# Kernel tuning notes

Measured on AMD Instinct MI355X. Metric: run time of the kernel, lower is better.

The kernel has to match this reference:

```python
import jax, jax.numpy as jnp
import numpy as np

IN_DIM, BANDS = 42, 22
H_VAD, H_NOISE, H_DEN = 24, 48, 96


def gru(x, w_ih, w_hh, b_ih, b_hh):
    """torch.nn.GRU (batch_first) semantics, h0=0.
    x: [B,T,D]; w_ih: [3H,D]; w_hh: [3H,H]; gate order r,z,n."""
    H = w_hh.shape[1]
    # precompute input projections for all timesteps (big GEMM, recurrence only on H)
    xp = jnp.einsum('btd,gd->btg', x, w_ih) + b_ih  # [B,T,3H]

    def step(h, xt):
        hp = h @ w_hh.T + b_hh
        xr, xz, xn = jnp.split(xt, 3, axis=-1)
        hr, hz, hn = jnp.split(hp, 3, axis=-1)
        r = jax.nn.sigmoid(xr + hr)
        z = jax.nn.sigmoid(xz + hz)
        n = jnp.tanh(xn + r * hn)
        h_new = (1.0 - z) * n + z * h
        return h_new, h_new

    h0 = jnp.zeros((x.shape[0], H), x.dtype)
    _, hs = jax.lax.scan(step, h0, jnp.swapaxes(xp, 0, 1))  # [T,B,H]
    return jnp.swapaxes(hs, 0, 1)  # [B,T,H]


def setup_inputs() -> dict:
    key = jax.random.key(0)
    ks = jax.random.split(key, 20)

    def w(k, shape, fan):
        return (jax.random.normal(k, shape, jnp.float32) / np.sqrt(fan)).astype(jnp.float32)

    B, T = 256, 2000
    d_noise_in = H_VAD + H_VAD + IN_DIM     # 90
    d_den_in = H_VAD + H_NOISE + IN_DIM     # 114
    return {
        'x': jax.random.normal(ks[0], (B, T, IN_DIM), jnp.float32),
        'in_w': w(ks[1], (H_VAD, IN_DIM), IN_DIM),
        'in_b': jnp.zeros((H_VAD,), jnp.float32),
        'vad_wih': w(ks[2], (3 * H_VAD, H_VAD), H_VAD),
        'vad_whh': w(ks[3], (3 * H_VAD, H_VAD), H_VAD),
        'vad_bih': jnp.zeros((3 * H_VAD,), jnp.float32),
        'vad_bhh': jnp.zeros((3 * H_VAD,), jnp.float32),
        'vad_out_w': w(ks[4], (1, H_VAD), H_VAD),
        'vad_out_b': jnp.zeros((1,), jnp.float32),
        'noise_wih': w(ks[5], (3 * H_NOISE, d_noise_in), d_noise_in),
        'noise_whh': w(ks[6], (3 * H_NOISE, H_NOISE), H_NOISE),
        'noise_bih': jnp.zeros((3 * H_NOISE,), jnp.float32),
        'noise_bhh': jnp.zeros((3 * H_NOISE,), jnp.float32),
        'den_wih': w(ks[7], (3 * H_DEN, d_den_in), d_den_in),
        'den_whh': w(ks[8], (3 * H_DEN, H_DEN), H_DEN),
        'den_bih': jnp.zeros((3 * H_DEN,), jnp.float32),
        'den_bhh': jnp.zeros((3 * H_DEN,), jnp.float32),
        'out_w': w(ks[9], (BANDS, H_DEN), H_DEN),
        'out_b': jnp.zeros((BANDS,), jnp.float32),
    }


def reference(x, in_w, in_b, vad_wih, vad_whh, vad_bih, vad_bhh,
              vad_out_w, vad_out_b, noise_wih, noise_whh, noise_bih, noise_bhh,
              den_wih, den_whh, den_bih, den_bhh, out_w, out_b):
    tmp = jnp.tanh(jnp.einsum('btd,hd->bth', x, in_w) + in_b)          # [B,T,24]
    vad_h = gru(tmp, vad_wih, vad_whh, vad_bih, vad_bhh)               # [B,T,24]
    vad = jax.nn.sigmoid(jnp.einsum('bth,oh->bto', vad_h, vad_out_w) + vad_out_b)
    noise_in = jnp.concatenate([tmp, vad_h, x], axis=-1)               # [B,T,90]
    noise_h = gru(noise_in, noise_wih, noise_whh, noise_bih, noise_bhh)  # [B,T,48]
    den_in = jnp.concatenate([vad_h, noise_h, x], axis=-1)             # [B,T,114]
    den_h = gru(den_in, den_wih, den_whh, den_bih, den_bhh)            # [B,T,96]
    gains = jax.nn.sigmoid(jnp.einsum('bth,oh->bto', den_h, out_w) + out_b)
    return gains, vad
```

## Files before the change

kernel.cpp:

```cpp
#include <hip/hip_runtime.h>

typedef _Float16 f16;
typedef _Float16 h2 __attribute__((ext_vector_type(2)));
typedef unsigned int u32;

#define TB  256
#define TTT 2000
#define INW 42
#define HV  24
#define HN  48
#define HD  96
#define NTH 640

__device__ __forceinline__ float fsigm(float v) {
    return __builtin_amdgcn_rcpf(1.0f + __builtin_amdgcn_exp2f(-1.44269504089f * v));
}
__device__ __forceinline__ float ftanh(float v) {
    float e = __builtin_amdgcn_exp2f(2.88539008178f * v);
    return 1.0f - 2.0f * __builtin_amdgcn_rcpf(e + 1.0f);
}
__device__ __forceinline__ float dot2f(u32 a, u32 w, float c) {
#if __has_builtin(__builtin_amdgcn_fdot2)
    return __builtin_amdgcn_fdot2(__builtin_bit_cast(h2, a), __builtin_bit_cast(h2, w), c, false);
#else
    h2 av = __builtin_bit_cast(h2, a), wv = __builtin_bit_cast(h2, w);
    return c + (float)av[0] * (float)wv[0] + (float)av[1] * (float)wv[1];
#endif
}
__device__ __forceinline__ u32 packw(float a, float b) {
    h2 v; v[0] = (f16)a; v[1] = (f16)b;
    return __builtin_bit_cast(u32, v);
}
template<int CTRL>
__device__ __forceinline__ float dpp_add(float x) {
    int y = __builtin_amdgcn_mov_dpp(__builtin_bit_cast(int, x), CTRL, 0xF, 0xF, true);
    return x + __builtin_bit_cast(float, y);
}

#define SYNCB() asm volatile("s_waitcnt lgkmcnt(0)\n\ts_barrier" ::: "memory")

#define ACCI(AV, W, IDX) do { u32 _a = (AV); \
    rr = dot2f(_a, W[0][IDX], rr); zz = dot2f(_a, W[1][IDX], zz); an = dot2f(_a, W[2][IDX], an); } while (0)
#define ACCH(AV, W, IDX) do { u32 _a = (AV); \
    rr = dot2f(_a, W[0][IDX], rr); zz = dot2f(_a, W[1][IDX], zz); hn = dot2f(_a, W[2][IDX], hn); } while (0)
#define RED4_Q() do { \
    rr = dpp_add<0xB1>(rr); rr = dpp_add<0x4E>(rr); \
    zz = dpp_add<0xB1>(zz); zz = dpp_add<0x4E>(zz); \
    an = dpp_add<0xB1>(an); an = dpp_add<0x4E>(an); \
    hn = dpp_add<0xB1>(hn); hn = dpp_add<0x4E>(hn); } while (0)
#define RED4_1() do { \
    rr = dpp_add<0xB1>(rr); zz = dpp_add<0xB1>(zz); \
    an = dpp_add<0xB1>(an); hn = dpp_add<0xB1>(hn); } while (0)

template<int N> struct IC { static constexpr int val = N; };

__global__ __launch_bounds__(NTH, 3) void rnnoise_kernel(
    const float* __restrict__ gx,
    const float* __restrict__ in_w,      const float* __restrict__ in_b,
    const float* __restrict__ vad_wih,   const float* __restrict__ vad_whh,
    const float* __restrict__ vad_bih,   const float* __restrict__ vad_bhh,
    const float* __restrict__ vad_out_w, const float* __restrict__ vad_out_b,
    const float* __restrict__ noise_wih, const float* __restrict__ noise_whh,
    const float* __restrict__ noise_bih, const float* __restrict__ noise_bhh,
    const float* __restrict__ den_wih,   const float* __restrict__ den_whh,
    const float* __restrict__ den_bih,   const float* __restrict__ den_bhh,
    const float* __restrict__ out_w,     const float* __restrict__ out_b,
    float* __restrict__ gains, float* __restrict__ vout)
{
    __shared__ __align__(16) f16 s_x[4][48];
    __shared__ __align__(16) f16 s_tmp[4][24];
    __shared__ __align__(16) f16 s_vadh[4][24];
    __shared__ __align__(16) f16 s_noih[4][48];
    __shared__ __align__(16) f16 s_denh[4][96];

    const int tid  = threadIdx.x;
    const int wid  = tid >> 6;
    const int lane = tid & 63;
    const int b    = blockIdx.x;

    if (tid < 96)  ((u32*)s_x)[tid]    = 0u;
    if (tid < 48)  ((u32*)s_tmp)[tid]  = 0u;
    if (tid < 48)  ((u32*)s_vadh)[tid] = 0u;
    if (tid < 96)  ((u32*)s_noih)[tid] = 0u;
    if (tid < 192) ((u32*)s_denh)[tid] = 0u;
    __syncthreads();

    const int role = (wid == 9) ? 2 : ((wid == 4 || wid == 5 || wid == 8) ? 1 : 0);

    if (role == 0) {
        const int dwi = (wid < 4) ? wid : (wid - 2);
        const int u = dwi * 16 + (lane >> 2), q = lane & 3;
        u32 wdh[3][12], wdx[3][6], wdv[3][3], wdn[3][6];
        #pragma unroll
        for (int g = 0; g < 3; ++g) {
            const float* wr = den_whh + (g * HD + u) * HD + 24 * q;
            #pragma unroll
            for (int j = 0; j < 12; ++j) wdh[g][j] = packw(wr[2*j], wr[2*j+1]);
            const float* wi = den_wih + (g * HD + u) * 114;
            #pragma unroll
            for (int j = 0; j < 6; ++j) {
                int c0 = 12*q + 2*j;
                float a = (c0     < INW) ? wi[72 + c0]     : 0.f;
                float c = (c0 + 1 < INW) ? wi[72 + c0 + 1] : 0.f;
                wdx[g][j] = packw(a, c);
            }
            #pragma unroll
            for (int j = 0; j < 3; ++j) wdv[g][j] = packw(wi[6*q + 2*j], wi[6*q + 2*j + 1]);
            #pragma unroll
            for (int j = 0; j < 6; ++j) wdn[g][j] = packw(wi[24 + 12*q + 2*j], wi[24 + 12*q + 2*j + 1]);
        }
        const float bdr  = den_bih[u]      + den_bhh[u];
        const float bdz  = den_bih[HD+u]   + den_bhh[HD+u];
        const float bdni = den_bih[2*HD+u];
        const float bdnh = den_bhh[2*HD+u];
        float hreg = 0.f;

        auto step = [&](auto PC, int k) {
            constexpr int P  = decltype(PC)::val;
            constexpr int SI = (P + 1) & 3;
            if (k >= 3 && k <= TTT + 2) {
                float rr = 0, zz = 0, an = 0, hn = 0;
                const uint4* hp = (const uint4*)&s_denh[P][24*q];
                #pragma unroll
                for (int v = 0; v < 3; ++v) {
                    uint4 a = hp[v];
                    ACCH(a.x, wdh, 4*v+0); ACCH(a.y, wdh, 4*v+1);
                    ACCH(a.z, wdh, 4*v+2); ACCH(a.w, wdh, 4*v+3);
                }
                const uint2* xp = (const uint2*)&s_x[SI][12*q];
                #pragma unroll
                for (int v = 0; v < 3; ++v) { uint2 a = xp[v]; ACCI(a.x, wdx, 2*v); ACCI(a.y, wdx, 2*v+1); }
                const u32* vp = (const u32*)&s_vadh[SI][6*q];
                #pragma unroll
                for (int v = 0; v < 3; ++v) ACCI(vp[v], wdv, v);
                const uint2* np = (const uint2*)&s_noih[SI][12*q];
                #pragma unroll
                for (int v = 0; v < 3; ++v) { uint2 a = np[v]; ACCI(a.x, wdn, 2*v); ACCI(a.y, wdn, 2*v+1); }
                RED4_Q();
                if (q == 0) {
                    float r = fsigm(rr + bdr);
                    float z = fsigm(zz + bdz);
                    float n = ftanh(an + bdni + r * (hn + bdnh));
                    hreg = z * (hreg - n) + n;
                    s_denh[SI][u] = (f16)hreg;
                }
            }
            SYNCB();
        };
        #pragma clang loop unroll(disable)
        for (int k0 = 0; k0 < TTT + 4; k0 += 4) {
            step(IC<0>{}, k0); step(IC<1>{}, k0+1); step(IC<2>{}, k0+2); step(IC<3>{}, k0+3);
        }

    } else if (role == 1) {
        const int nwi = (wid == 4) ? 0 : ((wid == 5) ? 1 : 2);
        const int L = nwi * 64 + lane, u = L >> 2, q = L & 3;
        const int o = L >> 3, s8 = L & 7;
        const int oc = (o < 22) ? o : 0;
        u32 wnh[3][6], wnt[3][3], wnv[3][3], wnx[3][6], wo[6];
        #pragma unroll
        for (int g = 0; g < 3; ++g) {
            const float* wr = noise_whh + (g * HN + u) * HN + 12 * q;
            #pragma unroll
            for (int j = 0; j < 6; ++j) wnh[g][j] = packw(wr[2*j], wr[2*j+1]);
            const float* wi = noise_wih + (g * HN + u) * 90;
            #pragma unroll
            for (int j = 0; j < 3; ++j) wnt[g][j] = packw(wi[6*q + 2*j], wi[6*q + 2*j + 1]);
            #pragma unroll
            for (int j = 0; j < 3; ++j) wnv[g][j] = packw(wi[24 + 6*q + 2*j], wi[24 + 6*q + 2*j + 1]);
            #pragma unroll
            for (int j = 0; j < 6; ++j) {
                int c0 = 12*q + 2*j;
                float a = (c0     < INW) ? wi[48 + c0]     : 0.f;
                float c = (c0 + 1 < INW) ? wi[48 + c0 + 1] : 0.f;
                wnx[g][j] = packw(a, c);
            }
        }
        #pragma unroll
        for (int j = 0; j < 6; ++j) wo[j] = packw(out_w[oc*HD + 12*s8 + 2*j], out_w[oc*HD + 12*s8 + 2*j + 1]);
        const float bnr  = noise_bih[u]    + noise_bhh[u];
        const float bnz  = noise_bih[HN+u] + noise_bhh[HN+u];
        const float bnni = noise_bih[2*HN+u];
        const float bnnh = noise_bhh[2*HN+u];
        const float bo   = out_b[oc];
        float hreg = 0.f;

        auto step = [&](auto PC, int k) {
            constexpr int P  = decltype(PC)::val;
            constexpr int SI = (P + 2) & 3;
            constexpr int SH = (P + 1) & 3;
            if (k >= 2 && k <= TTT + 1) {
                float rr = 0, zz = 0, an = 0, hn = 0;
                const uint2* hp = (const uint2*)&s_noih[SH][12*q];
                #pragma unroll
                for (int v = 0; v < 3; ++v) { uint2 a = hp[v]; ACCH(a.x, wnh, 2*v); ACCH(a.y, wnh, 2*v+1); }
                const u32* tp = (const u32*)&s_tmp[SI][6*q];
                #pragma unroll
                for (int v = 0; v < 3; ++v) ACCI(tp[v], wnt, v);
                const u32* vp = (const u32*)&s_vadh[SI][6*q];
                #pragma unroll
                for (int v = 0; v < 3; ++v) ACCI(vp[v], wnv, v);
                const uint2* xp = (const uint2*)&s_x[SI][12*q];
                #pragma unroll
                for (int v = 0; v < 3; ++v) { uint2 a = xp[v]; ACCI(a.x, wnx, 2*v); ACCI(a.y, wnx, 2*v+1); }
                RED4_Q();
                if (q == 0) {
                    float r = fsigm(rr + bnr);
                    float z = fsigm(zz + bnz);
                    float n = ftanh(an + bnni + r * (hn + bnnh));
                    hreg = z * (hreg - n) + n;
                    s_noih[SI][u] = (f16)hreg;
                }
            }
            if (k >= 4) {
                float acc = 0;
                const uint2* dp = (const uint2*)&s_denh[P][12*s8];
                #pragma unroll
                for (int v = 0; v < 3; ++v) {
                    uint2 a = dp[v];
                    acc = dot2f(a.x, wo[2*v], acc); acc = dot2f(a.y, wo[2*v+1], acc);
                }
                acc = dpp_add<0xB1>(acc); acc = dpp_add<0x4E>(acc);
                acc += __shfl_xor(acc, 4);
                if (s8 == 0 && o < 22)
                    gains[((size_t)b * TTT + (k - 4)) * 22 + o] = fsigm(acc + bo);
            }
            SYNCB();
        };
        #pragma clang loop unroll(disable)
        for (int k0 = 0; k0 < TTT + 4; k0 += 4) {
            step(IC<0>{}, k0); step(IC<1>{}, k0+1); step(IC<2>{}, k0+2); step(IC<3>{}, k0+3);
        }

    } else {
        const int l = lane;
        const int u = (l < 48) ? (l >> 1) : 0, q2 = l & 1;
        u32 wvi[3][6], wvh[3][6], wtm[12];
        float bvr = 0, bvz = 0, bvni = 0, bvnh = 0, btm = 0, wvo_u = 0;
        if (l < 48) {
            #pragma unroll
            for (int g = 0; g < 3; ++g) {
                const float* wi = vad_wih + (g * HV + u) * HV + 12 * q2;
                const float* wh = vad_whh + (g * HV + u) * HV + 12 * q2;
                #pragma unroll
                for (int j = 0; j < 6; ++j) {
                    wvi[g][j] = packw(wi[2*j], wi[2*j+1]);
                    wvh[g][j] = packw(wh[2*j], wh[2*j+1]);
                }
            }
            #pragma unroll
            for (int j = 0; j < 12; ++j) {
                int c0 = 24*q2 + 2*j;
                float a = (c0     < INW) ? in_w[u*INW + c0]     : 0.f;
                float c = (c0 + 1 < INW) ? in_w[u*INW + c0 + 1] : 0.f;
                wtm[j] = packw(a, c);
            }
            bvr  = vad_bih[u]      + vad_bhh[u];
            bvz  = vad_bih[HV+u]   + vad_bhh[HV+u];
            bvni = vad_bih[2*HV+u];
            bvnh = vad_bhh[2*HV+u];
            btm  = in_b[u];
            if (q2 == 0) wvo_u = vad_out_w[u];
        }
        const float bvo = vad_out_b[0];
        float hreg = 0.f;

        float xa = 0, xb = 0, xc = 0, xd = 0;
        if (l < INW) {
            xa = gx[((size_t)b * TTT + 0) * INW + l];
            xb = gx[((size_t)b * TTT + 1) * INW + l];
            xc = gx[((size_t)b * TTT + 2) * INW + l];
            xd = gx[((size_t)b * TTT + 3) * INW + l];
        }

        auto step = [&](auto PC, int k) {
            constexpr int P  = decltype(PC)::val;
            constexpr int ST = (P + 3) & 3;
            constexpr int SH = (P + 2) & 3;
            if (k < TTT && l < INW) {
                float xv;
                if constexpr (P == 0) xv = xa; else if constexpr (P == 1) xv = xb;
                else if constexpr (P == 2) xv = xc; else xv = xd;
                s_x[P][l] = (f16)xv;
            }
            if (k + 4 < TTT && l < INW) {
                float xv = gx[((size_t)b * TTT + (k + 4)) * INW + l];
                if constexpr (P == 0) xa = xv; else if constexpr (P == 1) xb = xv;
                else if constexpr (P == 2) xc = xv; else xd = xv;
            }
            if (k >= 1 && k <= TTT) {
                float rr = 0, zz = 0, an = 0, hn = 0;
                if (l < 48) {
                    const uint2* tp = (const uint2*)&s_tmp[ST][12*q2];
                    const uint2* hp = (const uint2*)&s_vadh[SH][12*q2];
                    #pragma unroll
                    for (int v = 0; v < 3; ++v) {
                        uint2 a = tp[v]; ACCI(a.x, wvi, 2*v); ACCI(a.y, wvi, 2*v+1);
                        uint2 h = hp[v]; ACCH(h.x, wvh, 2*v); ACCH(h.y, wvh, 2*v+1);
                    }
                    RED4_1();
                    if (q2 == 0) {
                        float r = fsigm(rr + bvr);
                        float z = fsigm(zz + bvz);
                        float n = ftanh(an + bvni + r * (hn + bvnh));
                        hreg = z * (hreg - n) + n;
                        s_vadh[ST][u] = (f16)hreg;
                    }
                }
                float val = (l < 48 && q2 == 0) ? (wvo_u * hreg) : 0.f;
                val = dpp_add<0xB1>(val); val = dpp_add<0x4E>(val);
                val += __shfl_xor(val, 4); val += __shfl_xor(val, 8);
                val += __shfl_xor(val, 16); val += __shfl_xor(val, 32);
                if (l == 0) vout[(size_t)b * TTT + (k - 1)] = fsigm(val + bvo);
            }
            if (k < TTT) {
                float acc = 0;
                if (l < 48) {
                    const uint4* xp = (const uint4*)&s_x[P][24*q2];
                    #pragma unroll
                    for (int v = 0; v < 3; ++v) {
                        uint4 a = xp[v];
                        acc = dot2f(a.x, wtm[4*v+0], acc); acc = dot2f(a.y, wtm[4*v+1], acc);
                        acc = dot2f(a.z, wtm[4*v+2], acc); acc = dot2f(a.w, wtm[4*v+3], acc);
                    }
                    acc = dpp_add<0xB1>(acc);
                    if (q2 == 0) s_tmp[P][u] = (f16)ftanh(acc + btm);
                }
            }
            SYNCB();
        };
        #pragma clang loop unroll(disable)
        for (int k0 = 0; k0 < TTT + 4; k0 += 4) {
            step(IC<0>{}, k0); step(IC<1>{}, k0+1); step(IC<2>{}, k0+2); step(IC<3>{}, k0+3);
        }
    }
}

extern "C" void kernel_launch(void* const* d_in, const int* in_sizes, int n_in,
                              void* d_out, int out_size, void* d_ws, size_t ws_size,
                              hipStream_t stream) {
    (void)in_sizes; (void)n_in; (void)d_ws; (void)ws_size; (void)out_size;
    const float* gx        = (const float*)d_in[0];
    const float* in_w      = (const float*)d_in[1];
    const float* in_b      = (const float*)d_in[2];
    const float* vad_wih   = (const float*)d_in[3];
    const float* vad_whh   = (const float*)d_in[4];
    const float* vad_bih   = (const float*)d_in[5];
    const float* vad_bhh   = (const float*)d_in[6];
    const float* vad_out_w = (const float*)d_in[7];
    const float* vad_out_b = (const float*)d_in[8];
    const float* noise_wih = (const float*)d_in[9];
    const float* noise_whh = (const float*)d_in[10];
    const float* noise_bih = (const float*)d_in[11];
    const float* noise_bhh = (const float*)d_in[12];
    const float* den_wih   = (const float*)d_in[13];
    const float* den_whh   = (const float*)d_in[14];
    const float* den_bih   = (const float*)d_in[15];
    const float* den_bhh   = (const float*)d_in[16];
    const float* out_w     = (const float*)d_in[17];
    const float* out_b     = (const float*)d_in[18];
    float* gains = (float*)d_out;
    float* vout  = (float*)d_out + (size_t)TB * (size_t)TTT * 22;

    rnnoise_kernel<<<dim3(TB), dim3(NTH), 0, stream>>>(
        gx, in_w, in_b, vad_wih, vad_whh, vad_bih, vad_bhh, vad_out_w, vad_out_b,
        noise_wih, noise_whh, noise_bih, noise_bhh, den_wih, den_whh, den_bih, den_bhh,
        out_w, out_b, gains, vout);
}
```

Before: 1.923 ms.

## Compute noise and denoise GRU gate projections with MFMA on unified activation buffer

The noise and denoise GRU steps now use 16x16x32 f16 MFMA instructions instead of per-lane fdot2 chains with DPP reductions. All activations move into one contiguous shared buffer so the concatenated input can be read as B-fragments, and the output gain projection moves from the noise waves into two denoise waves, also on MFMA. The MFMA B operand is a single batch column broadcast across 16 columns, so most of the matrix work is redundant, and launch bounds drop to one block per SM to make room for the larger register weight fragments.

After: 2.364 ms. 1.23x slower.

```diff
diff --git a/kernel.cpp b/kernel.cpp
--- a/kernel.cpp
+++ b/kernel.cpp
@@ -2,6 +2,8 @@
 
 typedef _Float16 f16;
 typedef _Float16 h2 __attribute__((ext_vector_type(2)));
+typedef _Float16 f16x8 __attribute__((ext_vector_type(8)));
+typedef float f32x4 __attribute__((ext_vector_type(4)));
 typedef unsigned int u32;
 
 #define TB  256
@@ -12,6 +14,13 @@
 #define HD  96
 #define NTH 640
 
+#define C_TMP 0
+#define C_VAD 24
+#define C_X   48
+#define C_NOI 96
+#define C_DEN 160
+#define ACTW  256
+
 __device__ __forceinline__ float fsigm(float v) {
     return __builtin_amdgcn_rcpf(1.0f + __builtin_amdgcn_exp2f(-1.44269504089f * v));
 }
@@ -39,22 +48,24 @@
 
 #define SYNCB() asm volatile("s_waitcnt lgkmcnt(0)\n\ts_barrier" ::: "memory")
 
+#define MFMA16(A, B, C) __builtin_amdgcn_mfma_f32_16x16x32_f16((A), (B), (C), 0, 0, 0)
+
 #define ACCI(AV, W, IDX) do { u32 _a = (AV); \
     rr = dot2f(_a, W[0][IDX], rr); zz = dot2f(_a, W[1][IDX], zz); an = dot2f(_a, W[2][IDX], an); } while (0)
 #define ACCH(AV, W, IDX) do { u32 _a = (AV); \
     rr = dot2f(_a, W[0][IDX], rr); zz = dot2f(_a, W[1][IDX], zz); hn = dot2f(_a, W[2][IDX], hn); } while (0)
-#define RED4_Q() do { \
-    rr = dpp_add<0xB1>(rr); rr = dpp_add<0x4E>(rr); \
-    zz = dpp_add<0xB1>(zz); zz = dpp_add<0x4E>(zz); \
-    an = dpp_add<0xB1>(an); an = dpp_add<0x4E>(an); \
-    hn = dpp_add<0xB1>(hn); hn = dpp_add<0x4E>(hn); } while (0)
 #define RED4_1() do { \
     rr = dpp_add<0xB1>(rr); zz = dpp_add<0xB1>(zz); \
     an = dpp_add<0xB1>(an); hn = dpp_add<0xB1>(hn); } while (0)
 
 template<int N> struct IC { static constexpr int val = N; };
 
-__global__ __launch_bounds__(NTH, 3) void rnnoise_kernel(
+__device__ __forceinline__ f16x8 ldsb(const f16* p) {
+    uint4 t = *(const uint4*)p;
+    return __builtin_bit_cast(f16x8, t);
+}
+
+__global__ __launch_bounds__(NTH, 1) void rnnoise_kernel(
     const float* __restrict__ gx,
     const float* __restrict__ in_w,      const float* __restrict__ in_b,
     const float* __restrict__ vad_wih,   const float* __restrict__ vad_whh,
@@ -67,82 +78,113 @@
     const float* __restrict__ out_w,     const float* __restrict__ out_b,
     float* __restrict__ gains, float* __restrict__ vout)
 {
-    __shared__ __align__(16) f16 s_x[4][48];
-    __shared__ __align__(16) f16 s_tmp[4][24];
-    __shared__ __align__(16) f16 s_vadh[4][24];
-    __shared__ __align__(16) f16 s_noih[4][48];
-    __shared__ __align__(16) f16 s_denh[4][96];
+    __shared__ __align__(16) f16 act[4][ACTW];
 
     const int tid  = threadIdx.x;
     const int wid  = tid >> 6;
     const int lane = tid & 63;
     const int b    = blockIdx.x;
-
-    if (tid < 96)  ((u32*)s_x)[tid]    = 0u;
-    if (tid < 48)  ((u32*)s_tmp)[tid]  = 0u;
-    if (tid < 48)  ((u32*)s_vadh)[tid] = 0u;
-    if (tid < 96)  ((u32*)s_noih)[tid] = 0u;
-    if (tid < 192) ((u32*)s_denh)[tid] = 0u;
-    __syncthreads();
+    const int g4   = lane >> 4;
+    const int rrow = lane & 15;
+
+    if (tid < 512) ((u32*)act)[tid] = 0u;
 
     const int role = (wid == 9) ? 2 : ((wid == 4 || wid == 5 || wid == 8) ? 1 : 0);
 
     if (role == 0) {
         const int dwi = (wid < 4) ? wid : (wid - 2);
-        const int u = dwi * 16 + (lane >> 2), q = lane & 3;
-        u32 wdh[3][12], wdx[3][6], wdv[3][3], wdn[3][6];
+        const int u_a = 16 * dwi + rrow;
+        f16x8 ag[3][7];
         #pragma unroll
         for (int g = 0; g < 3; ++g) {
-            const float* wr = den_whh + (g * HD + u) * HD + 24 * q;
+            const float* wi = den_wih + (g * HD + u_a) * 114;
+            const float* wh = den_whh + (g * HD + u_a) * HD;
             #pragma unroll
-            for (int j = 0; j < 12; ++j) wdh[g][j] = packw(wr[2*j], wr[2*j+1]);
-            const float* wi = den_wih + (g * HD + u) * 114;
+            for (int kt = 0; kt < 7; ++kt) {
+                #pragma unroll
+                for (int j = 0; j < 8; ++j) {
+                    int k = (kt < 4) ? (32 * kt + 8 * g4 + j) : (128 + 32 * (kt - 4) + 8 * g4 + j);
+                    float w = 0.f;
+                    if (k < 24)        w = wi[k];
+                    else if (k < 66)   w = wi[72 + (k - 24)];
+                    else if (k < 72)   w = 0.f;
+                    else if (k < 120)  w = wi[24 + (k - 72)];
+                    else if (k < 128)  w = 0.f;
+                    else               w = wh[k - 128];
+                    ag[g][kt][j] = (f16)w;
+                }
+            }
+        }
+        f16x8 ao0 = {}, ao1 = {}, ao2 = {};
+        if (dwi < 2) {
+            int o = 16 * dwi + rrow;
             #pragma unroll
-            for (int j = 0; j < 6; ++j) {
-                int c0 = 12*q + 2*j;
-                float a = (c0     < INW) ? wi[72 + c0]     : 0.f;
-                float c = (c0 + 1 < INW) ? wi[72 + c0 + 1] : 0.f;
-                wdx[g][j] = packw(a, c);
-            }
-            #pragma unroll
-            for (int j = 0; j < 3; ++j) wdv[g][j] = packw(wi[6*q + 2*j], wi[6*q + 2*j + 1]);
-            #pragma unroll
-            for (int j = 0; j < 6; ++j) wdn[g][j] = packw(wi[24 + 12*q + 2*j], wi[24 + 12*q + 2*j + 1]);
-        }
-        const float bdr  = den_bih[u]      + den_bhh[u];
-        const float bdz  = den_bih[HD+u]   + den_bhh[HD+u];
-        const float bdni = den_bih[2*HD+u];
-        const float bdnh = den_bhh[2*HD+u];
-        float hreg = 0.f;
+            for (int j = 0; j < 8; ++j) {
+                ao0[j] = (f16)((o < 22) ? out_w[o * HD +  0 + 8 * g4 + j] : 0.f);
+                ao1[j] = (f16)((o < 22) ? out_w[o * HD + 32 + 8 * g4 + j] : 0.f);
+                ao2[j] = (f16)((o < 22) ? out_w[o * HD + 64 + 8 * g4 + j] : 0.f);
+            }
+        }
+        float bdr[4], bdz[4], bdni[4], bdnh[4], bog[4];
+        #pragma unroll
+        for (int i = 0; i < 4; ++i) {
+            int u = 16 * dwi + 4 * g4 + i;
+            bdr[i]  = den_bih[u]        + den_bhh[u];
+            bdz[i]  = den_bih[HD + u]   + den_bhh[HD + u];
+            bdni[i] = den_bih[2*HD + u];
+            bdnh[i] = den_bhh[2*HD + u];
+            int o = 16 * dwi + 4 * g4 + i;
+            bog[i] = (dwi < 2 && o < 22) ? out_b[o] : 0.f;
+        }
+        float hprev[4] = {0.f, 0.f, 0.f, 0.f};
+        __syncthreads();
 
         auto step = [&](auto PC, int k) {
             constexpr int P  = decltype(PC)::val;
             constexpr int SI = (P + 1) & 3;
+            f16x8 bh0 = ldsb(&act[P][C_DEN +  0 + 8 * g4]);
+            f16x8 bh1 = ldsb(&act[P][C_DEN + 32 + 8 * g4]);
+            f16x8 bh2 = ldsb(&act[P][C_DEN + 64 + 8 * g4]);
             if (k >= 3 && k <= TTT + 2) {
-                float rr = 0, zz = 0, an = 0, hn = 0;
-                const uint4* hp = (const uint4*)&s_denh[P][24*q];
-                #pragma unroll
-                for (int v = 0; v < 3; ++v) {
-                    uint4 a = hp[v];
-                    ACCH(a.x, wdh, 4*v+0); ACCH(a.y, wdh, 4*v+1);
-                    ACCH(a.z, wdh, 4*v+2); ACCH(a.w, wdh, 4*v+3);
-                }
-                const uint2* xp = (const uint2*)&s_x[SI][12*q];
-                #pragma unroll
-                for (int v = 0; v < 3; ++v) { uint2 a = xp[v]; ACCI(a.x, wdx, 2*v); ACCI(a.y, wdx, 2*v+1); }
-                const u32* vp = (const u32*)&s_vadh[SI][6*q];
-                #pragma unroll
-                for (int v = 0; v < 3; ++v) ACCI(vp[v], wdv, v);
-                const uint2* np = (const uint2*)&s_noih[SI][12*q];
-                #pragma unroll
-                for (int v = 0; v < 3; ++v) { uint2 a = np[v]; ACCI(a.x, wdn, 2*v); ACCI(a.y, wdn, 2*v+1); }
-                RED4_Q();
-                if (q == 0) {
-                    float r = fsigm(rr + bdr);
-                    float z = fsigm(zz + bdz);
-                    float n = ftanh(an + bdni + r * (hn + bdnh));
-                    hreg = z * (hreg - n) + n;
-                    s_denh[SI][u] = (f16)hreg;
+                f16x8 b0 = ldsb(&act[SI][24 +  0 + 8 * g4]);
+                f16x8 b1 = ldsb(&act[SI][24 + 32 + 8 * g4]);
+                f16x8 b2 = ldsb(&act[SI][24 + 64 + 8 * g4]);
+                f16x8 b3 = ldsb(&act[SI][24 + 96 + 8 * g4]);
+                f32x4 aR = {0,0,0,0}, aZ = {0,0,0,0}, aNi = {0,0,0,0}, aNh = {0,0,0,0};
+                aR = MFMA16(ag[0][0], b0, aR); aZ = MFMA16(ag[1][0], b0, aZ); aNi = MFMA16(ag[2][0], b0, aNi);
+                aR = MFMA16(ag[0][1], b1, aR); aZ = MFMA16(ag[1][1], b1, aZ); aNi = MFMA16(ag[2][1], b1, aNi);
+                aR = MFMA16(ag[0][2], b2, aR); aZ = MFMA16(ag[1][2], b2, aZ); aNi = MFMA16(ag[2][2], b2, aNi);
+                aR = MFMA16(ag[0][3], b3, aR); aZ = MFMA16(ag[1][3], b3, aZ); aNi = MFMA16(ag[2][3], b3, aNi);
+                aR = MFMA16(ag[0][4], bh0, aR); aZ = MFMA16(ag[1][4], bh0, aZ); aNh = MFMA16(ag[2][4], bh0, aNh);
+                aR = MFMA16(ag[0][5], bh1, aR); aZ = MFMA16(ag[1][5], bh1, aZ); aNh = MFMA16(ag[2][5], bh1, aNh);
+                aR = MFMA16(ag[0][6], bh2, aR); aZ = MFMA16(ag[1][6], bh2, aZ); aNh = MFMA16(ag[2][6], bh2, aNh);
+                #pragma unroll
+                for (int i = 0; i < 4; ++i) {
+                    float r = fsigm(aR[i] + bdr[i]);
+                    float z = fsigm(aZ[i] + bdz[i]);
+                    float n = ftanh(aNi[i] + bdni[i] + r * (aNh[i] + bdnh[i]));
+                    hprev[i] = z * (hprev[i] - n) + n;
+                }
+                if ((lane & 15) == 0) {
+                    h2 p0, p1;
+                    p0[0] = (f16)hprev[0]; p0[1] = (f16)hprev[1];
+                    p1[0] = (f16)hprev[2]; p1[1] = (f16)hprev[3];
+                    uint2 w; w.x = __builtin_bit_cast(u32, p0); w.y = __builtin_bit_cast(u32, p1);
+                    *(uint2*)&act[SI][C_DEN + 16 * dwi + 4 * g4] = w;
+                }
+            }
+            if (dwi < 2 && k >= 4) {
+                f32x4 aO = {0,0,0,0};
+                aO = MFMA16(ao0, bh0, aO);
+                aO = MFMA16(ao1, bh1, aO);
+                aO = MFMA16(ao2, bh2, aO);
+                if ((lane & 15) == 0) {
+                    #pragma unroll
+                    for (int i = 0; i < 4; ++i) {
+                        int o = 16 * dwi + 4 * g4 + i;
+                        if (o < 22)
+                            gains[((size_t)b * TTT + (k - 4)) * 22 + o] = fsigm(aO[i] + bog[i]);
+                    }
                 }
             }
             SYNCB();
@@ -154,76 +196,68 @@
 
     } else if (role == 1) {
         const int nwi = (wid == 4) ? 0 : ((wid == 5) ? 1 : 2);
-        const int L = nwi * 64 + lane, u = L >> 2, q = L & 3;
-        const int o = L >> 3, s8 = L & 7;
-        const int oc = (o < 22) ? o : 0;
-        u32 wnh[3][6], wnt[3][3], wnv[3][3], wnx[3][6], wo[6];
+        const int u_a = 16 * nwi + rrow;
+        f16x8 ag[3][5];
         #pragma unroll
         for (int g = 0; g < 3; ++g) {
-            const float* wr = noise_whh + (g * HN + u) * HN + 12 * q;
+            const float* wi = noise_wih + (g * HN + u_a) * 90;
+            const float* wh = noise_whh + (g * HN + u_a) * HN;
             #pragma unroll
-            for (int j = 0; j < 6; ++j) wnh[g][j] = packw(wr[2*j], wr[2*j+1]);
-            const float* wi = noise_wih + (g * HN + u) * 90;
-            #pragma unroll
-            for (int j = 0; j < 3; ++j) wnt[g][j] = packw(wi[6*q + 2*j], wi[6*q + 2*j + 1]);
-            #pragma unroll
-            for (int j = 0; j < 3; ++j) wnv[g][j] = packw(wi[24 + 6*q + 2*j], wi[24 + 6*q + 2*j + 1]);
-            #pragma unroll
-            for (int j = 0; j < 6; ++j) {
-                int c0 = 12*q + 2*j;
-                float a = (c0     < INW) ? wi[48 + c0]     : 0.f;
-                float c = (c0 + 1 < INW) ? wi[48 + c0 + 1] : 0.f;
-                wnx[g][j] = packw(a, c);
-            }
-        }
+            for (int kt = 0; kt < 5; ++kt) {
+                #pragma unroll
+                for (int j = 0; j < 8; ++j) {
+                    int k = (kt < 3) ? (32 * kt + 8 * g4 + j) : (96 + 32 * (kt - 3) + 8 * g4 + j);
+                    float w = 0.f;
+                    if (k < 90)       w = wi[k];
+                    else if (k < 96)  w = 0.f;
+                    else if (k < 144) w = wh[k - 96];
+                    else              w = 0.f;
+                    ag[g][kt][j] = (f16)w;
+                }
+            }
+        }
+        float bnr[4], bnz[4], bnni[4], bnnh[4];
         #pragma unroll
-        for (int j = 0; j < 6; ++j) wo[j] = packw(out_w[oc*HD + 12*s8 + 2*j], out_w[oc*HD + 12*s8 + 2*j + 1]);
-        const float bnr  = noise_bih[u]    + noise_bhh[u];
-        const float bnz  = noise_bih[HN+u] + noise_bhh[HN+u];
-        const float bnni = noise_bih[2*HN+u];
-        const float bnnh = noise_bhh[2*HN+u];
-        const float bo   = out_b[oc];
-        float hreg = 0.f;
+        for (int i = 0; i < 4; ++i) {
+            int u = 16 * nwi + 4 * g4 + i;
+            bnr[i]  = noise_bih[u]        + noise_bhh[u];
+            bnz[i]  = noise_bih[HN + u]   + noise_bhh[HN + u];
+            bnni[i] = noise_bih[2*HN + u];
+            bnnh[i] = noise_bhh[2*HN + u];
+        }
+        float hprev[4] = {0.f, 0.f, 0.f, 0.f};
+        __syncthreads();
 
         auto step = [&](auto PC, int k) {
-            constexpr int P  = decltype(PC)::val;
-            constexpr int SI = (P + 2) & 3;
-            constexpr int SH = (P + 1) & 3;
+            constexpr int P   = decltype(PC)::val;
+            constexpr int SI2 = (P + 2) & 3;
+            constexpr int SH  = (P + 1) & 3;
             if (k >= 2 && k <= TTT + 1) {
-                float rr = 0, zz = 0, an = 0, hn = 0;
-                const uint2* hp = (const uint2*)&s_noih[SH][12*q];
-                #pragma unroll
-                for (int v = 0; v < 3; ++v) { uint2 a = hp[v]; ACCH(a.x, wnh, 2*v); ACCH(a.y, wnh, 2*v+1); }
-                const u32* tp = (const u32*)&s_tmp[SI][6*q];
-                #pragma unroll
-                for (int v = 0; v < 3; ++v) ACCI(tp[v], wnt, v);
-                const u32* vp = (const u32*)&s_vadh[SI][6*q];
-                #pragma unroll
-                for (int v = 0; v < 3; ++v) ACCI(vp[v], wnv, v);
-                const uint2* xp = (const uint2*)&s_x[SI][12*q];
-                #pragma unroll
-                for (int v = 0; v < 3; ++v) { uint2 a = xp[v]; ACCI(a.x, wnx, 2*v); ACCI(a.y, wnx, 2*v+1); }
-                RED4_Q();
-                if (q == 0) {
-                    float r = fsigm(rr + bnr);
-                    float z = fsigm(zz + bnz);
-                    float n = ftanh(an + bnni + r * (hn + bnnh));
-                    hreg = z * (hreg - n) + n;
-                    s_noih[SI][u] = (f16)hreg;
-                }
-            }
-            if (k >= 4) {
-                float acc = 0;
-                const uint2* dp = (const uint2*)&s_denh[P][12*s8];
-                #pragma unroll
-                for (int v = 0; v < 3; ++v) {
-                    uint2 a = dp[v];
-                    acc = dot2f(a.x, wo[2*v], acc); acc = dot2f(a.y, wo[2*v+1], acc);
-                }
-                acc = dpp_add<0xB1>(acc); acc = dpp_add<0x4E>(acc);
-                acc += __shfl_xor(acc, 4);
-                if (s8 == 0 && o < 22)
-                    gains[((size_t)b * TTT + (k - 4)) * 22 + o] = fsigm(acc + bo);
+                f16x8 b0  = ldsb(&act[SI2][ 0 + 8 * g4]);
+                f16x8 b1  = ldsb(&act[SI2][32 + 8 * g4]);
+                f16x8 b2  = ldsb(&act[SI2][64 + 8 * g4]);
+                f16x8 bh0 = ldsb(&act[SH][C_NOI +  0 + 8 * g4]);
+                f16x8 bh1 = ldsb(&act[SH][C_NOI + 32 + 8 * g4]);
+                f32x4 aR = {0,0,0,0}, aZ = {0,0,0,0}, aNi = {0,0,0,0}, aNh = {0,0,0,0};
+                aR = MFMA16(ag[0][0], b0, aR); aZ = MFMA16(ag[1][0], b0, aZ); aNi = MFMA16(ag[2][0], b0, aNi);
+                aR = MFMA16(ag[0][1], b1, aR); aZ = MFMA16(ag[1][1], b1, aZ); aNi = MFMA16(ag[2][1], b1, aNi);
+                aR = MFMA16(ag[0][2], b2, aR); aZ = MFMA16(ag[1][2], b2, aZ); aNi = MFMA16(ag[2][2], b2, aNi);
+                aR = MFMA16(ag[0][3], bh0, aR); aZ = MFMA16(ag[1][3], bh0, aZ); aNh = MFMA16(ag[2][3], bh0, aNh);
+                aR = MFMA16(ag[0][4], bh1, aR); aZ = MFMA16(ag[1][4], bh1, aZ); aNh = MFMA16(ag[2][4], bh1, aNh);
+                #pragma unroll
+                for (int i = 0; i < 4; ++i) {
+                    float r = fsigm(aR[i] + bnr[i]);
+                    float z = fsigm(aZ[i] + bnz[i]);
+                    float n = ftanh(aNi[i] + bnni[i] + r * (aNh[i] + bnnh[i]));
+                    hprev[i] = z * (hprev[i] - n) + n;
+                }
+                if ((lane & 15) == 0) {
+                    h2 p0, p1;
+                    p0[0] = (f16)hprev[0]; p0[1] = (f16)hprev[1];
+                    p1[0] = (f16)hprev[2]; p1[1] = (f16)hprev[3];
+                    uint2 w; w.x = __builtin_bit_cast(u32, p0); w.y = __builtin_bit_cast(u32, p1);
+                    *(uint2*)&act[SI2][C_NOI + 16 * nwi + 4 * g4] = w;
+                }
             }
             SYNCB();
         };
@@ -250,15 +284,15 @@
             }
             #pragma unroll
             for (int j = 0; j < 12; ++j) {
-                int c0 = 24*q2 + 2*j;
-                float a = (c0     < INW) ? in_w[u*INW + c0]     : 0.f;
-                float c = (c0 + 1 < INW) ? in_w[u*INW + c0 + 1] : 0.f;
+                int c0 = 24 * q2 + 2 * j;
+                float a = (c0     < INW) ? in_w[u * INW + c0]     : 0.f;
+                float c = (c0 + 1 < INW) ? in_w[u * INW + c0 + 1] : 0.f;
                 wtm[j] = packw(a, c);
             }
-            bvr  = vad_bih[u]      + vad_bhh[u];
-            bvz  = vad_bih[HV+u]   + vad_bhh[HV+u];
-            bvni = vad_bih[2*HV+u];
-            bvnh = vad_bhh[2*HV+u];
+            bvr  = vad_bih[u]        + vad_bhh[u];
+            bvz  = vad_bih[HV + u]   + vad_bhh[HV + u];
+            bvni = vad_bih[2*HV + u];
+            bvnh = vad_bhh[2*HV + u];
             btm  = in_b[u];
             if (q2 == 0) wvo_u = vad_out_w[u];
         }
@@ -272,6 +306,7 @@
             xc = gx[((size_t)b * TTT + 2) * INW + l];
             xd = gx[((size_t)b * TTT + 3) * INW + l];
         }
+        __syncthreads();
 
         auto step = [&](auto PC, int k) {
             constexpr int P  = decltype(PC)::val;
@@ -281,7 +316,7 @@
                 float xv;
                 if constexpr (P == 0) xv = xa; else if constexpr (P == 1) xv = xb;
                 else if constexpr (P == 2) xv = xc; else xv = xd;
-                s_x[P][l] = (f16)xv;
+                act[P][C_X + l] = (f16)xv;
             }
             if (k + 4 < TTT && l < INW) {
                 float xv = gx[((size_t)b * TTT + (k + 4)) * INW + l];
@@ -291,8 +326,8 @@
             if (k >= 1 && k <= TTT) {
                 float rr = 0, zz = 0, an = 0, hn = 0;
                 if (l < 48) {
-                    const uint2* tp = (const uint2*)&s_tmp[ST][12*q2];
-                    const uint2* hp = (const uint2*)&s_vadh[SH][12*q2];
+                    const uint2* tp = (const uint2*)&act[ST][C_TMP + 12 * q2];
+                    const uint2* hp = (const uint2*)&act[SH][C_VAD + 12 * q2];
                     #pragma unroll
                     for (int v = 0; v < 3; ++v) {
                         uint2 a = tp[v]; ACCI(a.x, wvi, 2*v); ACCI(a.y, wvi, 2*v+1);
@@ -304,7 +339,7 @@
                         float z = fsigm(zz + bvz);
                         float n = ftanh(an + bvni + r * (hn + bvnh));
                         hreg = z * (hreg - n) + n;
-                        s_vadh[ST][u] = (f16)hreg;
+                        act[ST][C_VAD + u] = (f16)hreg;
                     }
                 }
                 float val = (l < 48 && q2 == 0) ? (wvo_u * hreg) : 0.f;
@@ -313,19 +348,17 @@
                 val += __shfl_xor(val, 16); val += __shfl_xor(val, 32);
                 if (l == 0) vout[(size_t)b * TTT + (k - 1)] = fsigm(val + bvo);
             }
-            if (k < TTT) {
+            if (k < TTT && l < 48) {
                 float acc = 0;
-                if (l < 48) {
-                    const uint4* xp = (const uint4*)&s_x[P][24*q2];
-                    #pragma unroll
-                    for (int v = 0; v < 3; ++v) {
-                        uint4 a = xp[v];
-                        acc = dot2f(a.x, wtm[4*v+0], acc); acc = dot2f(a.y, wtm[4*v+1], acc);
-                        acc = dot2f(a.z, wtm[4*v+2], acc); acc = dot2f(a.w, wtm[4*v+3], acc);
-                    }
-                    acc = dpp_add<0xB1>(acc);
-                    if (q2 == 0) s_tmp[P][u] = (f16)ftanh(acc + btm);
-                }
+                const uint4* xp = (const uint4*)&act[P][C_X + 24 * q2];
+                #pragma unroll
+                for (int v = 0; v < 3; ++v) {
+                    uint4 a = xp[v];
+                    acc = dot2f(a.x, wtm[4*v+0], acc); acc = dot2f(a.y, wtm[4*v+1], acc);
+                    acc = dot2f(a.z, wtm[4*v+2], acc); acc = dot2f(a.w, wtm[4*v+3], acc);
+                }
+                acc = dpp_add<0xB1>(acc);
+                if (q2 == 0) act[P][C_TMP + u] = (f16)ftanh(acc + btm);
             }
             SYNCB();
         };
```
